# Optimization experiments

Measured on AMD Instinct MI355X. Metric: run time of the kernel, lower is better.

The kernel has to match this reference:

```python
import jax, jax.numpy as jnp
import numpy as np

B, T, E, D, G = 64, 64, 2048, 4096, 8
H3 = 3 * D  # gru projects deter -> 3*deter (reset, cand, update)
EPS = 1e-4  # Norm default eps


def _rms(x, scale):
    # Norm impl='rms': x * rsqrt(mean(x^2, -1) + eps) * scale
    return x * (jax.lax.rsqrt((x * x).mean(-1, keepdims=True) + EPS) * scale)


def setup_inputs() -> dict:
    key = jax.random.key(0)
    ks = jax.random.split(key, 4)
    x = jax.random.normal(ks[0], (B, T, E), jnp.float32)
    deter0 = jax.random.normal(ks[1], (B, D), jnp.float32)
    # dense in-projection: concat(deter, x) -> D, rms norm + silu
    W_in = jax.random.normal(ks[2], (D + E, D), jnp.float32) * (1.0 / np.sqrt(D + E))
    b_in = jnp.zeros((D,), jnp.float32)
    scale_in = jnp.ones((D,), jnp.float32)
    # BlockLinear D -> 3D with G groups; weight (G, D/G, 3D/G), per-block rms scales
    W_blk = jax.random.normal(ks[3], (G, D // G, H3 // G), jnp.float32) * (1.0 / np.sqrt(D // G))
    b_blk = jnp.zeros((H3,), jnp.float32)
    scale_blk = jnp.ones((G, H3 // G), jnp.float32)
    return dict(x=x, deter0=deter0, W_in=W_in, b_in=b_in, scale_in=scale_in,
                W_blk=W_blk, b_blk=b_blk, scale_blk=scale_blk)


def reference(x, deter0, W_in, b_in, scale_in, W_blk, b_blk, scale_blk):
    def step(deter, x_t):
        h = jnp.concatenate([deter, x_t], -1)                # [B, D+E]
        y = jax.nn.silu(_rms(h @ W_in + b_in, scale_in))     # [B, D]
        # block-diagonal GEMM: '...ki,kio->...ko' as in BlockLinear._layer
        z = jnp.einsum('bgi,gio->bgo', y.reshape(B, G, D // G), W_blk)
        z = z.reshape(B, H3) + b_blk
        # block_norm=True: per-block rms over each of the G contiguous chunks
        z = _rms(z.reshape(B, G, H3 // G), scale_blk).reshape(B, H3)
        reset, cand, update = jnp.split(z, 3, -1)
        reset = jax.nn.sigmoid(reset)
        cand = jnp.tanh(reset * cand)
        update = jax.nn.sigmoid(update - 1.0)
        deter = update * cand + (1.0 - update) * deter
        return deter, deter

    _, deters = jax.lax.scan(step, deter0, jnp.swapaxes(x, 0, 1))  # scan over T
    return jnp.swapaxes(deters, 0, 1)  # [B, T, D]
```

## Files before the change

### kernel.cpp

```cpp
#include <hip/hip_runtime.h>

typedef unsigned short u16;
typedef unsigned int u32;
typedef __bf16 bfx8 __attribute__((ext_vector_type(8)));
typedef float f32x4 __attribute__((ext_vector_type(4)));

constexpr int BB = 64;
constexpr int TT = 64;
constexpr int EE = 2048;
constexpr int DD = 4096;
constexpr int GG = 8;
constexpr int H3 = 3 * DD;
constexpr int CH = H3 / GG;
constexpr float EPSf = 1e-4f;

static __device__ __forceinline__ u16 f2bf(float f) {
  u32 u = __builtin_bit_cast(u32, f);
  u32 r = (u + 0x7fffu + ((u >> 16) & 1u)) >> 16;
  return (u16)r;
}
static __device__ __forceinline__ float bf2f(u16 h) {
  return __builtin_bit_cast(float, (u32)h << 16);
}


__global__ void __launch_bounds__(256) k_f2b(const float* __restrict__ in,
                                             u16* __restrict__ out, int n4) {
  int i = blockIdx.x * 256 + threadIdx.x;
  int stride = gridDim.x * 256;
  for (; i < n4; i += stride) {
    float4 v = ((const float4*)in)[i];
    uint2 o;
    o.x = (u32)f2bf(v.x) | ((u32)f2bf(v.y) << 16);
    o.y = (u32)f2bf(v.z) | ((u32)f2bf(v.w) << 16);
    ((uint2*)out)[i] = o;
  }
}

__global__ void __launch_bounds__(256) k_initdet(const float* __restrict__ d0,
                                                 float* __restrict__ dF,
                                                 u16* __restrict__ dB, int n4) {
  int i = blockIdx.x * 256 + threadIdx.x;
  if (i < n4) {
    float4 v = ((const float4*)d0)[i];
    ((float4*)dF)[i] = v;
    uint2 o;
    o.x = (u32)f2bf(v.x) | ((u32)f2bf(v.y) << 16);
    o.y = (u32)f2bf(v.z) | ((u32)f2bf(v.w) << 16);
    ((uint2*)dB)[i] = o;
  }
}

__global__ void __launch_bounds__(256) k_transpose_f2b(const float* __restrict__ in,
                                                       u16* __restrict__ out,
                                                       int R, int C) {
  __shared__ float tile[32][33];
  size_t base = (size_t)blockIdx.z * R * C;
  in += base; out += base;
  int tx = threadIdx.x & 31, ty = threadIdx.x >> 5;
  int r0 = blockIdx.y * 32, c0 = blockIdx.x * 32;
#pragma unroll
  for (int i = 0; i < 4; i++) {
    int rr = ty * 4 + i;
    tile[rr][tx] = in[(size_t)(r0 + rr) * C + (c0 + tx)];
  }
  __syncthreads();
#pragma unroll
  for (int i = 0; i < 4; i++) {
    int cc = ty * 4 + i;
    out[(size_t)(c0 + cc) * R + (r0 + tx)] = f2bf(tile[tx][cc]);
  }
}

constexpr int P1_LS = 72;
constexpr int P1_BUF = 128 * P1_LS;

__global__ void __launch_bounds__(256) k_p1(const u16* __restrict__ A,
                                            const u16* __restrict__ B,
                                            const float* __restrict__ bias,
                                            u16* __restrict__ C) {
  __shared__ u16 As[2 * P1_BUF];
  __shared__ u16 Bs[2 * P1_BUF];
  const int tid = threadIdx.x;
  const int m0 = blockIdx.y * 128, n0 = blockIdx.x * 128;
  const int w = tid >> 6, lane = tid & 63;
  const int wr = w >> 1, wc = w & 1;
  const int lr = lane & 15, lk = (lane >> 4) * 8, rq = (lane >> 4) * 4;
  const int srow = tid >> 3, scol = (tid & 7) * 8;
  const u16* Ag = A + (size_t)(m0 + srow) * EE + scol;
  const u16* Bg = B + (size_t)(n0 + srow) * (DD + EE) + scol;

  f32x4 acc[4][4] = {};
  uint4 ra[4], rb[4];
#pragma unroll
  for (int i = 0; i < 4; i++) {
    ra[i] = *(const uint4*)(Ag + (size_t)32 * i * EE);
    rb[i] = *(const uint4*)(Bg + (size_t)32 * i * (DD + EE));
  }

  for (int kt = 0; kt < 32; ++kt) {
    const int p = kt & 1;
    u16* ab = As + p * P1_BUF;
    u16* bb = Bs + p * P1_BUF;
#pragma unroll
    for (int i = 0; i < 4; i++) {
      *(uint4*)&ab[(srow + 32 * i) * P1_LS + scol] = ra[i];
      *(uint4*)&bb[(srow + 32 * i) * P1_LS + scol] = rb[i];
    }
    __syncthreads();
    if (kt < 31) {
      const int ko = (kt + 1) * 64;
#pragma unroll
      for (int i = 0; i < 4; i++) {
        ra[i] = *(const uint4*)(Ag + (size_t)32 * i * EE + ko);
        rb[i] = *(const uint4*)(Bg + (size_t)32 * i * (DD + EE) + ko);
      }
    }
#pragma unroll
    for (int kk = 0; kk < 64; kk += 32) {
      bfx8 av[4], bv[4];
#pragma unroll
      for (int mi = 0; mi < 4; mi++)
        av[mi] = *(const bfx8*)&ab[(wr * 64 + mi * 16 + lr) * P1_LS + kk + lk];
#pragma unroll
      for (int ni = 0; ni < 4; ni++)
        bv[ni] = *(const bfx8*)&bb[(wc * 64 + ni * 16 + lr) * P1_LS + kk + lk];
#pragma unroll
      for (int mi = 0; mi < 4; mi++)
#pragma unroll
        for (int ni = 0; ni < 4; ni++)
          acc[mi][ni] = __builtin_amdgcn_mfma_f32_16x16x32_bf16(av[mi], bv[ni], acc[mi][ni], 0, 0, 0);
    }
  }

#pragma unroll
  for (int mi = 0; mi < 4; mi++) {
#pragma unroll
    for (int ni = 0; ni < 4; ni++) {
      const int n = n0 + wc * 64 + ni * 16 + lr;
      const float bias_v = bias[n];
#pragma unroll
      for (int r = 0; r < 4; r++) {
        const int m = m0 + wr * 64 + mi * 16 + rq + r;
        C[(size_t)m * DD + n] = f2bf(acc[mi][ni][r] + bias_v);
      }
    }
  }
}

constexpr int LSA = 136;
constexpr int ABUF = 64 * LSA;

__global__ void __launch_bounds__(512) kA(const u16* __restrict__ dB,
                                          const u16* __restrict__ WT,
                                          float* __restrict__ part) {
  __shared__ u16 As[2 * ABUF];
  __shared__ u16 Bs[2 * ABUF];
  const int tid = threadIdx.x;
  const int n0 = blockIdx.x * 64;
  const int k0 = blockIdx.y * 1024;
  const int w = tid >> 6, lane = tid & 63;
  const int wr = w >> 1, wc = w & 1;
  const int lr = lane & 15, lk = (lane >> 4) * 8, rq = (lane >> 4) * 4;
  const int r0s = tid >> 4, s0 = (tid & 15) * 8;
  const int r1s = r0s + 32;
  const u16* Ag0 = dB + (size_t)r0s * DD + k0 + s0;
  const u16* Ag1 = dB + (size_t)r1s * DD + k0 + s0;
  const u16* Bg0 = WT + (size_t)(n0 + r0s) * (DD + EE) + k0 + s0;
  const u16* Bg1 = WT + (size_t)(n0 + r1s) * (DD + EE) + k0 + s0;
  const int d0 = r0s * LSA + s0, d1 = r1s * LSA + s0;

  f32x4 acc[2] = {};
  uint4 ra0 = *(const uint4*)(Ag0);
  uint4 ra1 = *(const uint4*)(Ag1);
  uint4 rb0 = *(const uint4*)(Bg0);
  uint4 rb1 = *(const uint4*)(Bg1);

  for (int kt = 0; kt < 8; ++kt) {
    const int p = kt & 1;
    u16* ab = As + p * ABUF;
    u16* bb = Bs + p * ABUF;
    *(uint4*)&ab[d0] = ra0;
    *(uint4*)&ab[d1] = ra1;
    *(uint4*)&bb[d0] = rb0;
    *(uint4*)&bb[d1] = rb1;
    __syncthreads();
    if (kt < 7) {
      const int ko = (kt + 1) * 128;
      ra0 = *(const uint4*)(Ag0 + ko);
      ra1 = *(const uint4*)(Ag1 + ko);
      rb0 = *(const uint4*)(Bg0 + ko);
      rb1 = *(const uint4*)(Bg1 + ko);
    }
#pragma unroll
    for (int kk = 0; kk < 128; kk += 32) {
      bfx8 av = *(const bfx8*)&ab[(wr * 16 + lr) * LSA + kk + lk];
#pragma unroll
      for (int ni = 0; ni < 2; ni++) {
        bfx8 bv = *(const bfx8*)&bb[(wc * 32 + ni * 16 + lr) * LSA + kk + lk];
        acc[ni] = __builtin_amdgcn_mfma_f32_16x16x32_bf16(av, bv, acc[ni], 0, 0, 0);
      }
    }
  }

  float* Pp = part + (size_t)blockIdx.y * BB * DD;
#pragma unroll
  for (int ni = 0; ni < 2; ni++)
#pragma unroll
    for (int r = 0; r < 4; r++)
      Pp[(size_t)(wr * 16 + rq + r) * DD + n0 + wc * 32 + ni * 16 + lr] = acc[ni][r];
}

__global__ void __launch_bounds__(256) kB(const float* __restrict__ part,
                                          const u16* __restrict__ Xproj,
                                          const float* __restrict__ scale_in,
                                          u16* __restrict__ ybf, int t) {
  const int b = blockIdx.x, tid = threadIdx.x;
  const int w = tid >> 6, lane = tid & 63;
  __shared__ float sred[4];
  const u16* xp = Xproj + ((size_t)b * TT + t) * DD + tid * 16;
  const float* pb = part + (size_t)b * DD + tid * 16;
  float v[16];
  uint4 x0 = *(const uint4*)(xp);
  uint4 x1 = *(const uint4*)(xp + 8);
#pragma unroll
  for (int j = 0; j < 8; j++) v[j] = bf2f(((const u16*)&x0)[j]);
#pragma unroll
  for (int j = 0; j < 8; j++) v[8 + j] = bf2f(((const u16*)&x1)[j]);
#pragma unroll
  for (int kc = 0; kc < 4; kc++) {
    const float* p = pb + (size_t)kc * BB * DD;
#pragma unroll
    for (int j4 = 0; j4 < 4; j4++) {
      float4 q = *(const float4*)(p + j4 * 4);
      v[j4 * 4 + 0] += q.x; v[j4 * 4 + 1] += q.y;
      v[j4 * 4 + 2] += q.z; v[j4 * 4 + 3] += q.w;
    }
  }
  float ss = 0.f;
#pragma unroll
  for (int j = 0; j < 16; j++) ss += v[j] * v[j];
#pragma unroll
  for (int o = 32; o > 0; o >>= 1) ss += __shfl_down(ss, o);
  if (lane == 0) sred[w] = ss;
  __syncthreads();
  const float r = rsqrtf((sred[0] + sred[1] + sred[2] + sred[3]) / (float)DD + EPSf);
  const float* sc = scale_in + tid * 16;
  uint2 o0, o1;
  u32* po = (u32*)&o0;
#pragma unroll
  for (int j = 0; j < 4; j++) {
    float a = v[2 * j] * r * sc[2 * j];
    float bq = v[2 * j + 1] * r * sc[2 * j + 1];
    a = a / (1.f + __expf(-a)); bq = bq / (1.f + __expf(-bq));
    po[j & 1] = (u32)f2bf(a) | ((u32)f2bf(bq) << 16);
    if (j == 1) *(uint2*)(ybf + (size_t)b * DD + tid * 16) = o0;
  }
  *(uint2*)(ybf + (size_t)b * DD + tid * 16 + 4) = o0;
  u32 pk[8];
#pragma unroll
  for (int j = 0; j < 8; j++) {
    float a = v[2 * j] * r * sc[2 * j];
    float bq = v[2 * j + 1] * r * sc[2 * j + 1];
    a = a / (1.f + __expf(-a)); bq = bq / (1.f + __expf(-bq));
    pk[j] = (u32)f2bf(a) | ((u32)f2bf(bq) << 16);
  }
  uint4 w0 = make_uint4(pk[0], pk[1], pk[2], pk[3]);
  uint4 w1 = make_uint4(pk[4], pk[5], pk[6], pk[7]);
  *(uint4*)(ybf + (size_t)b * DD + tid * 16) = w0;
  *(uint4*)(ybf + (size_t)b * DD + tid * 16 + 8) = w1;
}

constexpr int LSC2 = 72;
constexpr int CBUF = 64 * LSC2;

__global__ void __launch_bounds__(256) kC(const u16* __restrict__ ybf,
                                          const u16* __restrict__ WbT,
                                          const float* __restrict__ b_blk,
                                          float* __restrict__ zbuf,
                                          float* __restrict__ zsq) {
  __shared__ u16 As[2 * CBUF];
  __shared__ u16 Bs[2 * CBUF];
  const int tid = threadIdx.x;
  const int wg = blockIdx.x;
  const int n0g = wg * 64;
  const int g = n0g / CH, nl = n0g % CH;
  const int w = tid >> 6, lane = tid & 63;
  const int lr = lane & 15, lk = (lane >> 4) * 8, rq = (lane >> 4) * 4;
  const int srow = tid >> 2, sc = (tid & 3) * 8;
  const u16* Arow = ybf + (size_t)srow * DD + g * (DD / GG) + sc;
  const u16* Brow = WbT + ((size_t)g * CH + nl + srow) * (DD / GG) + sc;
  const int dA = srow * LSC2 + sc;

  f32x4 acc[4] = {};
  uint4 ra0 = *(const uint4*)(Arow);
  uint4 ra1 = *(const uint4*)(Arow + 32);
  uint4 rb0 = *(const uint4*)(Brow);
  uint4 rb1 = *(const uint4*)(Brow + 32);

  for (int kt = 0; kt < 8; ++kt) {
    const int p = kt & 1;
    u16* ab = As + p * CBUF;
    u16* bb = Bs + p * CBUF;
    *(uint4*)&ab[dA] = ra0;
    *(uint4*)&ab[dA + 32] = ra1;
    *(uint4*)&bb[dA] = rb0;
    *(uint4*)&bb[dA + 32] = rb1;
    __syncthreads();
    if (kt < 7) {
      const int ko = (kt + 1) * 64;
      ra0 = *(const uint4*)(Arow + ko);
      ra1 = *(const uint4*)(Arow + ko + 32);
      rb0 = *(const uint4*)(Brow + ko);
      rb1 = *(const uint4*)(Brow + ko + 32);
    }
#pragma unroll
    for (int kk = 0; kk < 64; kk += 32) {
      bfx8 av = *(const bfx8*)&ab[(w * 16 + lr) * LSC2 + kk + lk];
#pragma unroll
      for (int ni = 0; ni < 4; ni++) {
        bfx8 bv = *(const bfx8*)&bb[(ni * 16 + lr) * LSC2 + kk + lk];
        acc[ni] = __builtin_amdgcn_mfma_f32_16x16x32_bf16(av, bv, acc[ni], 0, 0, 0);
      }
    }
  }

  float sq[4] = {0.f, 0.f, 0.f, 0.f};
#pragma unroll
  for (int ni = 0; ni < 4; ni++) {
    const int n = n0g + ni * 16 + lr;
    const float bias_v = b_blk[n];
#pragma unroll
    for (int r = 0; r < 4; r++) {
      const float zv = acc[ni][r] + bias_v;
      zbuf[(size_t)(w * 16 + rq + r) * H3 + n] = zv;
      sq[r] += zv * zv;
    }
  }
#pragma unroll
  for (int o = 1; o < 16; o <<= 1) {
#pragma unroll
    for (int r = 0; r < 4; r++) sq[r] += __shfl_xor(sq[r], o);
  }
  if (lr == 0) {
#pragma unroll
    for (int r = 0; r < 4; r++) zsq[(size_t)wg * 64 + w * 16 + rq + r] = sq[r];
  }
}

__global__ void __launch_bounds__(256) kD(const float* __restrict__ zbuf,
                                          const float* __restrict__ zsq,
                                          const float* __restrict__ sblk,
                                          float* __restrict__ dF,
                                          u16* __restrict__ dB,
                                          float* __restrict__ out, int t) {
  const int wg = blockIdx.x, tid = threadIdx.x;
  const int b = wg >> 2, s = wg & 3;
  __shared__ float sred[8];
  if (tid < 8) {
    float ssq = 0.f;
    const int j0 = tid * 24;
#pragma unroll
    for (int j = 0; j < 24; j++) ssq += zsq[(size_t)(j0 + j) * 64 + b];
    sred[tid] = rsqrtf(ssq / (float)CH + EPSf);
  }
  __syncthreads();
  const int d0 = s * 1024 + tid * 4;
  const float* zr = zbuf + (size_t)b * H3;
  float4 z0 = *(const float4*)(zr + d0);
  float4 z1 = *(const float4*)(zr + DD + d0);
  float4 z2 = *(const float4*)(zr + 2 * DD + d0);
  float4 dold = *(const float4*)(dF + (size_t)b * DD + d0);
  const float rsA = sred[d0 / CH];
  const float rsB = sred[(DD + d0) / CH];
  const float rsC = sred[(2 * DD + d0) / CH];
  float dn[4];
  const float* z0p = (const float*)&z0;
  const float* z1p = (const float*)&z1;
  const float* z2p = (const float*)&z2;
  const float* dop = (const float*)&dold;
#pragma unroll
  for (int e = 0; e < 4; e++) {
    const int dd = d0 + e;
    const float a0 = z0p[e] * rsA * sblk[dd];
    const float a1 = z1p[e] * rsB * sblk[DD + dd];
    const float a2 = z2p[e] * rsC * sblk[2 * DD + dd];
    const float reset = 1.f / (1.f + __expf(-a0));
    const float cand = tanhf(reset * a1);
    const float upd = 1.f / (1.f + __expf(-(a2 - 1.f)));
    dn[e] = upd * cand + (1.f - upd) * dop[e];
  }
  *(float4*)(dF + (size_t)b * DD + d0) = make_float4(dn[0], dn[1], dn[2], dn[3]);
  uint2 o;
  o.x = (u32)f2bf(dn[0]) | ((u32)f2bf(dn[1]) << 16);
  o.y = (u32)f2bf(dn[2]) | ((u32)f2bf(dn[3]) << 16);
  *(uint2*)(dB + (size_t)b * DD + d0) = o;
  *(float4*)(out + ((size_t)b * TT + t) * DD + d0) = make_float4(dn[0], dn[1], dn[2], dn[3]);
}


extern "C" void kernel_launch(void* const* d_in, const int* in_sizes, int n_in,
                              void* d_out, int out_size, void* d_ws, size_t ws_size,
                              hipStream_t stream) {
  (void)in_sizes; (void)n_in; (void)out_size; (void)ws_size;
  const float* x         = (const float*)d_in[0];
  const float* deter0    = (const float*)d_in[1];
  const float* W_in      = (const float*)d_in[2];
  const float* b_in      = (const float*)d_in[3];
  const float* scale_in  = (const float*)d_in[4];
  const float* W_blk     = (const float*)d_in[5];
  const float* b_blk     = (const float*)d_in[6];
  const float* scale_blk = (const float*)d_in[7];
  float* out = (float*)d_out;

  char* ws = (char*)d_ws;
  size_t off = 0;
  auto alloc = [&](size_t bytes) -> void* {
    void* p = ws + off;
    off += (bytes + 255) & ~(size_t)255;
    return p;
  };
  u16*   WT    = (u16*)alloc((size_t)DD * (DD + EE) * 2);
  u16*   WbT   = (u16*)alloc((size_t)GG * CH * (DD / GG) * 2);
  u16*   Xproj = (u16*)alloc((size_t)BB * TT * DD * 2);
  float* dF    = (float*)alloc((size_t)BB * DD * 4);
  u16*   dB    = (u16*)alloc((size_t)BB * DD * 2);
  char* scratch = (char*)alloc((size_t)BB * TT * EE * 2);
  u16*   xbf  = (u16*)scratch;
  float* part = (float*)scratch;
  size_t o2 = (size_t)4 * BB * DD * 4;
  u16*   ybf  = (u16*)(scratch + o2);
  o2 += (size_t)BB * DD * 2;
  float* zbuf = (float*)(scratch + o2);
  o2 += (size_t)BB * H3 * 4;
  float* zsq  = (float*)(scratch + o2);

  k_f2b<<<dim3(2048), dim3(256), 0, stream>>>(x, xbf, BB * TT * EE / 4);
  k_transpose_f2b<<<dim3(DD / 32, (DD + EE) / 32, 1), dim3(256), 0, stream>>>(W_in, WT, DD + EE, DD);
  k_transpose_f2b<<<dim3(CH / 32, (DD / GG) / 32, GG), dim3(256), 0, stream>>>(W_blk, WbT, DD / GG, CH);
  k_initdet<<<dim3(BB * DD / 4 / 256), dim3(256), 0, stream>>>(deter0, dF, dB, BB * DD / 4);

  k_p1<<<dim3(DD / 128, BB * TT / 128), dim3(256), 0, stream>>>(
      xbf, WT + DD, b_in, Xproj);

  for (int t = 0; t < TT; t++) {
    kA<<<dim3(64, 4), dim3(512), 0, stream>>>(dB, WT, part);
    kB<<<dim3(BB), dim3(256), 0, stream>>>(part, Xproj, scale_in, ybf, t);
    kC<<<dim3(192), dim3(256), 0, stream>>>(ybf, WbT, b_blk, zbuf, zsq);
    kD<<<dim3(256), dim3(256), 0, stream>>>(zbuf, zsq, scale_blk, dF, dB, out, t);
  }
}
```

Baseline: 1.999 ms.

## Fuse recurrent step kernels pairwise using in-kernel grid barriers

```diff
diff --git a/kernel.cpp b/kernel.cpp
--- a/kernel.cpp
+++ b/kernel.cpp
@@ -2,6 +2,7 @@
 
 typedef unsigned short u16;
 typedef unsigned int u32;
+typedef unsigned long long u64;
 typedef __bf16 bfx8 __attribute__((ext_vector_type(8)));
 typedef float f32x4 __attribute__((ext_vector_type(4)));
 
@@ -21,6 +22,35 @@
 }
 static __device__ __forceinline__ float bf2f(u16 h) {
   return __builtin_bit_cast(float, (u32)h << 16);
+}
+
+static __device__ __forceinline__ uint2 ld_dev2(const void* p) {
+  u64 v = __hip_atomic_load((const u64*)p, __ATOMIC_RELAXED, __HIP_MEMORY_SCOPE_AGENT);
+  uint2 r; r.x = (u32)v; r.y = (u32)(v >> 32);
+  return r;
+}
+static __device__ __forceinline__ float ld_devf(const float* p) {
+  return __hip_atomic_load(p, __ATOMIC_RELAXED, __HIP_MEMORY_SCOPE_AGENT);
+}
+static __device__ __forceinline__ void st_devf(float* p, float v) {
+  __hip_atomic_store(p, v, __ATOMIC_RELAXED, __HIP_MEMORY_SCOPE_AGENT);
+}
+static __device__ __forceinline__ float2 u2f2(uint2 v) {
+  float2 r;
+  r.x = __builtin_bit_cast(float, v.x);
+  r.y = __builtin_bit_cast(float, v.y);
+  return r;
+}
+
+static __device__ __forceinline__ void gbar(int* cnt, int target) {
+  __syncthreads();
+  if (threadIdx.x == 0) {
+    __hip_atomic_fetch_add(cnt, 1, __ATOMIC_RELAXED, __HIP_MEMORY_SCOPE_AGENT);
+    while (__hip_atomic_load(cnt, __ATOMIC_RELAXED, __HIP_MEMORY_SCOPE_AGENT) < target)
+      __builtin_amdgcn_s_sleep(2);
+  }
+  __syncthreads();
+  asm volatile("" ::: "memory");
 }
 
 
@@ -49,6 +79,11 @@
     o.y = (u32)f2bf(v.z) | ((u32)f2bf(v.w) << 16);
     ((uint2*)dB)[i] = o;
   }
+}
+
+__global__ void __launch_bounds__(256) k_zero(int* __restrict__ p, int n) {
+  int i = blockIdx.x * 256 + threadIdx.x;
+  if (i < n) p[i] = 0;
 }
 
 __global__ void __launch_bounds__(256) k_transpose_f2b(const float* __restrict__ in,
@@ -151,251 +186,276 @@
 constexpr int LSA = 136;
 constexpr int ABUF = 64 * LSA;
 
-__global__ void __launch_bounds__(512) kA(const u16* __restrict__ dB,
-                                          const u16* __restrict__ WT,
-                                          float* __restrict__ part) {
+__global__ void __launch_bounds__(512) kAB(const u16* __restrict__ dB,
+                                           const u16* __restrict__ WT,
+                                           const u16* __restrict__ Xproj,
+                                           const float* __restrict__ scale_in,
+                                           float* __restrict__ part,
+                                           u16* __restrict__ ybf,
+                                           int t, int* bar) {
   __shared__ u16 As[2 * ABUF];
   __shared__ u16 Bs[2 * ABUF];
-  const int tid = threadIdx.x;
-  const int n0 = blockIdx.x * 64;
-  const int k0 = blockIdx.y * 1024;
-  const int w = tid >> 6, lane = tid & 63;
-  const int wr = w >> 1, wc = w & 1;
-  const int lr = lane & 15, lk = (lane >> 4) * 8, rq = (lane >> 4) * 4;
-  const int r0s = tid >> 4, s0 = (tid & 15) * 8;
-  const int r1s = r0s + 32;
-  const u16* Ag0 = dB + (size_t)r0s * DD + k0 + s0;
-  const u16* Ag1 = dB + (size_t)r1s * DD + k0 + s0;
-  const u16* Bg0 = WT + (size_t)(n0 + r0s) * (DD + EE) + k0 + s0;
-  const u16* Bg1 = WT + (size_t)(n0 + r1s) * (DD + EE) + k0 + s0;
-  const int d0 = r0s * LSA + s0, d1 = r1s * LSA + s0;
-
-  f32x4 acc[2] = {};
-  uint4 ra0 = *(const uint4*)(Ag0);
-  uint4 ra1 = *(const uint4*)(Ag1);
-  uint4 rb0 = *(const uint4*)(Bg0);
-  uint4 rb1 = *(const uint4*)(Bg1);
-
-  for (int kt = 0; kt < 8; ++kt) {
-    const int p = kt & 1;
-    u16* ab = As + p * ABUF;
-    u16* bb = Bs + p * ABUF;
-    *(uint4*)&ab[d0] = ra0;
-    *(uint4*)&ab[d1] = ra1;
-    *(uint4*)&bb[d0] = rb0;
-    *(uint4*)&bb[d1] = rb1;
+  __shared__ float sred[8];
+  __shared__ u16 occupancy_pad[8192];
+  const int wg = blockIdx.x, tid = threadIdx.x;
+  if ((int)blockIdx.y == -1) occupancy_pad[0] = 1;
+
+  {
+    const int n0 = (wg & 63) * 64;
+    const int k0 = (wg >> 6) * 1024;
+    const int w = tid >> 6, lane = tid & 63;
+    const int wr = w >> 1, wc = w & 1;
+    const int lr = lane & 15, lk = (lane >> 4) * 8, rq = (lane >> 4) * 4;
+    const int r0s = tid >> 4, s0 = (tid & 15) * 8;
+    const u16* Ag0 = dB + (size_t)r0s * DD + k0 + s0;
+    const u16* Ag1 = dB + (size_t)(r0s + 32) * DD + k0 + s0;
+    const u16* Bg0 = WT + (size_t)(n0 + r0s) * (DD + EE) + k0 + s0;
+    const u16* Bg1 = WT + (size_t)(n0 + r0s + 32) * (DD + EE) + k0 + s0;
+    const int d0 = r0s * LSA + s0, d1 = (r0s + 32) * LSA + s0;
+    u16* A0 = As;        u16* B0 = Bs;
+    u16* A1 = As + ABUF; u16* B1 = Bs + ABUF;
+
+    f32x4 acc[2] = {};
+    uint4 ea0 = *(const uint4*)(Ag0),      ea1 = *(const uint4*)(Ag1);
+    uint4 eb0 = *(const uint4*)(Bg0),      eb1 = *(const uint4*)(Bg1);
+    uint4 oa0 = *(const uint4*)(Ag0 + 128), oa1 = *(const uint4*)(Ag1 + 128);
+    uint4 ob0 = *(const uint4*)(Bg0 + 128), ob1 = *(const uint4*)(Bg1 + 128);
+
+#pragma unroll
+    for (int it = 0; it < 4; ++it) {
+      *(uint4*)&A0[d0] = ea0; *(uint4*)&A0[d1] = ea1;
+      *(uint4*)&B0[d0] = eb0; *(uint4*)&B0[d1] = eb1;
+      __syncthreads();
+      if (it < 3) {
+        const int ko = (2 * it + 2) * 128;
+        ea0 = *(const uint4*)(Ag0 + ko); ea1 = *(const uint4*)(Ag1 + ko);
+        eb0 = *(const uint4*)(Bg0 + ko); eb1 = *(const uint4*)(Bg1 + ko);
+      }
+#pragma unroll
+      for (int kk = 0; kk < 128; kk += 32) {
+        bfx8 av = *(const bfx8*)&A0[(wr * 16 + lr) * LSA + kk + lk];
+#pragma unroll
+        for (int ni = 0; ni < 2; ni++) {
+          bfx8 bv = *(const bfx8*)&B0[(wc * 32 + ni * 16 + lr) * LSA + kk + lk];
+          acc[ni] = __builtin_amdgcn_mfma_f32_16x16x32_bf16(av, bv, acc[ni], 0, 0, 0);
+        }
+      }
+      *(uint4*)&A1[d0] = oa0; *(uint4*)&A1[d1] = oa1;
+      *(uint4*)&B1[d0] = ob0; *(uint4*)&B1[d1] = ob1;
+      __syncthreads();
+      if (it < 3) {
+        const int ko = (2 * it + 3) * 128;
+        oa0 = *(const uint4*)(Ag0 + ko); oa1 = *(const uint4*)(Ag1 + ko);
+        ob0 = *(const uint4*)(Bg0 + ko); ob1 = *(const uint4*)(Bg1 + ko);
+      }
+#pragma unroll
+      for (int kk = 0; kk < 128; kk += 32) {
+        bfx8 av = *(const bfx8*)&A1[(wr * 16 + lr) * LSA + kk + lk];
+#pragma unroll
+        for (int ni = 0; ni < 2; ni++) {
+          bfx8 bv = *(const bfx8*)&B1[(wc * 32 + ni * 16 + lr) * LSA + kk + lk];
+          acc[ni] = __builtin_amdgcn_mfma_f32_16x16x32_bf16(av, bv, acc[ni], 0, 0, 0);
+        }
+      }
+    }
+
+    float* Pp = part + (size_t)(wg >> 6) * BB * DD;
+#pragma unroll
+    for (int ni = 0; ni < 2; ni++)
+#pragma unroll
+      for (int r = 0; r < 4; r++)
+        st_devf(&Pp[(size_t)(wr * 16 + rq + r) * DD + n0 + wc * 32 + ni * 16 + lr],
+                acc[ni][r]);
+  }
+
+  gbar(bar, 256);
+
+  if (wg < BB) {
+    const int b = wg;
+    const int w = tid >> 6, lane = tid & 63;
+    const u16* xp = Xproj + ((size_t)b * TT + t) * DD + tid * 8;
+    const float* pb = part + (size_t)b * DD + tid * 8;
+    float v[8];
+    uint4 x0 = *(const uint4*)(xp);
+#pragma unroll
+    for (int j = 0; j < 8; j++) v[j] = bf2f(((const u16*)&x0)[j]);
+#pragma unroll
+    for (int kc = 0; kc < 4; kc++) {
+      const float* p = pb + (size_t)kc * BB * DD;
+#pragma unroll
+      for (int j2 = 0; j2 < 4; j2++) {
+        float2 q = u2f2(ld_dev2(p + j2 * 2));
+        v[j2 * 2] += q.x;
+        v[j2 * 2 + 1] += q.y;
+      }
+    }
+    float ss = 0.f;
+#pragma unroll
+    for (int j = 0; j < 8; j++) ss += v[j] * v[j];
+#pragma unroll
+    for (int o = 32; o > 0; o >>= 1) ss += __shfl_down(ss, o);
+    if (lane == 0) sred[w] = ss;
     __syncthreads();
-    if (kt < 7) {
-      const int ko = (kt + 1) * 128;
-      ra0 = *(const uint4*)(Ag0 + ko);
-      ra1 = *(const uint4*)(Ag1 + ko);
-      rb0 = *(const uint4*)(Bg0 + ko);
-      rb1 = *(const uint4*)(Bg1 + ko);
-    }
-#pragma unroll
-    for (int kk = 0; kk < 128; kk += 32) {
-      bfx8 av = *(const bfx8*)&ab[(wr * 16 + lr) * LSA + kk + lk];
-#pragma unroll
-      for (int ni = 0; ni < 2; ni++) {
-        bfx8 bv = *(const bfx8*)&bb[(wc * 32 + ni * 16 + lr) * LSA + kk + lk];
-        acc[ni] = __builtin_amdgcn_mfma_f32_16x16x32_bf16(av, bv, acc[ni], 0, 0, 0);
-      }
-    }
-  }
-
-  float* Pp = part + (size_t)blockIdx.y * BB * DD;
-#pragma unroll
-  for (int ni = 0; ni < 2; ni++)
-#pragma unroll
-    for (int r = 0; r < 4; r++)
-      Pp[(size_t)(wr * 16 + rq + r) * DD + n0 + wc * 32 + ni * 16 + lr] = acc[ni][r];
-}
-
-__global__ void __launch_bounds__(256) kB(const float* __restrict__ part,
-                                          const u16* __restrict__ Xproj,
-                                          const float* __restrict__ scale_in,
-                                          u16* __restrict__ ybf, int t) {
-  const int b = blockIdx.x, tid = threadIdx.x;
-  const int w = tid >> 6, lane = tid & 63;
-  __shared__ float sred[4];
-  const u16* xp = Xproj + ((size_t)b * TT + t) * DD + tid * 16;
-  const float* pb = part + (size_t)b * DD + tid * 16;
-  float v[16];
-  uint4 x0 = *(const uint4*)(xp);
-  uint4 x1 = *(const uint4*)(xp + 8);
-#pragma unroll
-  for (int j = 0; j < 8; j++) v[j] = bf2f(((const u16*)&x0)[j]);
-#pragma unroll
-  for (int j = 0; j < 8; j++) v[8 + j] = bf2f(((const u16*)&x1)[j]);
-#pragma unroll
-  for (int kc = 0; kc < 4; kc++) {
-    const float* p = pb + (size_t)kc * BB * DD;
-#pragma unroll
-    for (int j4 = 0; j4 < 4; j4++) {
-      float4 q = *(const float4*)(p + j4 * 4);
-      v[j4 * 4 + 0] += q.x; v[j4 * 4 + 1] += q.y;
-      v[j4 * 4 + 2] += q.z; v[j4 * 4 + 3] += q.w;
-    }
-  }
-  float ss = 0.f;
-#pragma unroll
-  for (int j = 0; j < 16; j++) ss += v[j] * v[j];
-#pragma unroll
-  for (int o = 32; o > 0; o >>= 1) ss += __shfl_down(ss, o);
-  if (lane == 0) sred[w] = ss;
-  __syncthreads();
-  const float r = rsqrtf((sred[0] + sred[1] + sred[2] + sred[3]) / (float)DD + EPSf);
-  const float* sc = scale_in + tid * 16;
-  uint2 o0, o1;
-  u32* po = (u32*)&o0;
-#pragma unroll
-  for (int j = 0; j < 4; j++) {
-    float a = v[2 * j] * r * sc[2 * j];
-    float bq = v[2 * j + 1] * r * sc[2 * j + 1];
-    a = a / (1.f + __expf(-a)); bq = bq / (1.f + __expf(-bq));
-    po[j & 1] = (u32)f2bf(a) | ((u32)f2bf(bq) << 16);
-    if (j == 1) *(uint2*)(ybf + (size_t)b * DD + tid * 16) = o0;
-  }
-  *(uint2*)(ybf + (size_t)b * DD + tid * 16 + 4) = o0;
-  u32 pk[8];
-#pragma unroll
-  for (int j = 0; j < 8; j++) {
-    float a = v[2 * j] * r * sc[2 * j];
-    float bq = v[2 * j + 1] * r * sc[2 * j + 1];
-    a = a / (1.f + __expf(-a)); bq = bq / (1.f + __expf(-bq));
-    pk[j] = (u32)f2bf(a) | ((u32)f2bf(bq) << 16);
-  }
-  uint4 w0 = make_uint4(pk[0], pk[1], pk[2], pk[3]);
-  uint4 w1 = make_uint4(pk[4], pk[5], pk[6], pk[7]);
-  *(uint4*)(ybf + (size_t)b * DD + tid * 16) = w0;
-  *(uint4*)(ybf + (size_t)b * DD + tid * 16 + 8) = w1;
+    float tot = 0.f;
+#pragma unroll
+    for (int i = 0; i < 8; i++) tot += sred[i];
+    const float r = rsqrtf(tot / (float)DD + EPSf);
+    const float* sc = scale_in + tid * 8;
+    u32 pk[4];
+#pragma unroll
+    for (int j = 0; j < 4; j++) {
+      float a = v[2 * j] * r * sc[2 * j];
+      float bq = v[2 * j + 1] * r * sc[2 * j + 1];
+      a = a / (1.f + __expf(-a));
+      bq = bq / (1.f + __expf(-bq));
+      pk[j] = (u32)f2bf(a) | ((u32)f2bf(bq) << 16);
+    }
+    *(uint4*)(ybf + (size_t)b * DD + tid * 8) = make_uint4(pk[0], pk[1], pk[2], pk[3]);
+  }
 }
 
 constexpr int LSC2 = 72;
 constexpr int CBUF = 64 * LSC2;
 
-__global__ void __launch_bounds__(256) kC(const u16* __restrict__ ybf,
-                                          const u16* __restrict__ WbT,
-                                          const float* __restrict__ b_blk,
-                                          float* __restrict__ zbuf,
-                                          float* __restrict__ zsq) {
+__global__ void __launch_bounds__(512) kCD(const u16* __restrict__ ybf,
+                                           const u16* __restrict__ WbT,
+                                           const float* __restrict__ b_blk,
+                                           const float* __restrict__ sblk,
+                                           float* __restrict__ zbuf,
+                                           float* __restrict__ zsq,
+                                           float* __restrict__ dF,
+                                           u16* __restrict__ dBout,
+                                           float* __restrict__ out,
+                                           int t, int* bar) {
   __shared__ u16 As[2 * CBUF];
   __shared__ u16 Bs[2 * CBUF];
-  const int tid = threadIdx.x;
-  const int wg = blockIdx.x;
-  const int n0g = wg * 64;
-  const int g = n0g / CH, nl = n0g % CH;
-  const int w = tid >> 6, lane = tid & 63;
-  const int lr = lane & 15, lk = (lane >> 4) * 8, rq = (lane >> 4) * 4;
-  const int srow = tid >> 2, sc = (tid & 3) * 8;
-  const u16* Arow = ybf + (size_t)srow * DD + g * (DD / GG) + sc;
-  const u16* Brow = WbT + ((size_t)g * CH + nl + srow) * (DD / GG) + sc;
-  const int dA = srow * LSC2 + sc;
-
-  f32x4 acc[4] = {};
-  uint4 ra0 = *(const uint4*)(Arow);
-  uint4 ra1 = *(const uint4*)(Arow + 32);
-  uint4 rb0 = *(const uint4*)(Brow);
-  uint4 rb1 = *(const uint4*)(Brow + 32);
-
-  for (int kt = 0; kt < 8; ++kt) {
-    const int p = kt & 1;
-    u16* ab = As + p * CBUF;
-    u16* bb = Bs + p * CBUF;
-    *(uint4*)&ab[dA] = ra0;
-    *(uint4*)&ab[dA + 32] = ra1;
-    *(uint4*)&bb[dA] = rb0;
-    *(uint4*)&bb[dA + 32] = rb1;
+  __shared__ float sred[8];
+  __shared__ u16 occupancy_pad[24576];
+  const int wg = blockIdx.x, tid = threadIdx.x;
+  if ((int)blockIdx.y == -1) occupancy_pad[0] = 1;
+
+  {
+    const int n0g = wg * 64;
+    const int g = wg / 24, nl = n0g - g * CH;
+    const int w = tid >> 6, lane = tid & 63;
+    const int wr = w >> 1, wc = w & 1;
+    const int lr = lane & 15, lk = (lane >> 4) * 8, rq = (lane >> 4) * 4;
+    const int srow = tid >> 3, sc = (tid & 7) * 8;
+    const u16* Arow = ybf + (size_t)srow * DD + g * 512 + sc;
+    const u16* Brow = WbT + ((size_t)g * CH + nl + srow) * 512 + sc;
+    const int dA = srow * LSC2 + sc;
+    u16* A0 = As;        u16* B0 = Bs;
+    u16* A1 = As + CBUF; u16* B1 = Bs + CBUF;
+
+    f32x4 acc[2] = {};
+    uint4 ea = *(const uint4*)(Arow),      eb = *(const uint4*)(Brow);
+    uint4 oa = *(const uint4*)(Arow + 64), ob = *(const uint4*)(Brow + 64);
+
+#pragma unroll
+    for (int it = 0; it < 4; ++it) {
+      *(uint4*)&A0[dA] = ea; *(uint4*)&B0[dA] = eb;
+      __syncthreads();
+      if (it < 3) {
+        const int ko = (2 * it + 2) * 64;
+        ea = *(const uint4*)(Arow + ko); eb = *(const uint4*)(Brow + ko);
+      }
+#pragma unroll
+      for (int kk = 0; kk < 64; kk += 32) {
+        bfx8 av = *(const bfx8*)&A0[(wr * 16 + lr) * LSC2 + kk + lk];
+#pragma unroll
+        for (int ni = 0; ni < 2; ni++) {
+          bfx8 bv = *(const bfx8*)&B0[(wc * 32 + ni * 16 + lr) * LSC2 + kk + lk];
+          acc[ni] = __builtin_amdgcn_mfma_f32_16x16x32_bf16(av, bv, acc[ni], 0, 0, 0);
+        }
+      }
+      *(uint4*)&A1[dA] = oa; *(uint4*)&B1[dA] = ob;
+      __syncthreads();
+      if (it < 3) {
+        const int ko = (2 * it + 3) * 64;
+        oa = *(const uint4*)(Arow + ko); ob = *(const uint4*)(Brow + ko);
+      }
+#pragma unroll
+      for (int kk = 0; kk < 64; kk += 32) {
+        bfx8 av = *(const bfx8*)&A1[(wr * 16 + lr) * LSC2 + kk + lk];
+#pragma unroll
+        for (int ni = 0; ni < 2; ni++) {
+          bfx8 bv = *(const bfx8*)&B1[(wc * 32 + ni * 16 + lr) * LSC2 + kk + lk];
+          acc[ni] = __builtin_amdgcn_mfma_f32_16x16x32_bf16(av, bv, acc[ni], 0, 0, 0);
+        }
+      }
+    }
+
+    float sq[4] = {0.f, 0.f, 0.f, 0.f};
+#pragma unroll
+    for (int ni = 0; ni < 2; ni++) {
+      const int n = n0g + wc * 32 + ni * 16 + lr;
+      const float bias_v = b_blk[n];
+#pragma unroll
+      for (int r = 0; r < 4; r++) {
+        const float zv = acc[ni][r] + bias_v;
+        st_devf(&zbuf[(size_t)(wr * 16 + rq + r) * H3 + n], zv);
+        sq[r] += zv * zv;
+      }
+    }
+#pragma unroll
+    for (int o = 1; o < 16; o <<= 1) {
+#pragma unroll
+      for (int r = 0; r < 4; r++) sq[r] += __shfl_xor(sq[r], o);
+    }
+    if (lr == 0) {
+#pragma unroll
+      for (int r = 0; r < 4; r++)
+        st_devf(&zsq[(size_t)wg * 128 + wc * 64 + wr * 16 + rq + r], sq[r]);
+    }
+  }
+
+  gbar(bar, 192);
+
+  if (wg < 128) {
+    const int b = wg >> 1, s = wg & 1;
+    if (tid < 8) {
+      float ssq = 0.f;
+      const int c0 = tid * 24;
+#pragma unroll
+      for (int j = 0; j < 24; j++) {
+        const size_t base = (size_t)(c0 + j) * 128;
+        ssq += ld_devf(&zsq[base + b]) + ld_devf(&zsq[base + 64 + b]);
+      }
+      sred[tid] = rsqrtf(ssq / (float)CH + EPSf);
+    }
     __syncthreads();
-    if (kt < 7) {
-      const int ko = (kt + 1) * 64;
-      ra0 = *(const uint4*)(Arow + ko);
-      ra1 = *(const uint4*)(Arow + ko + 32);
-      rb0 = *(const uint4*)(Brow + ko);
-      rb1 = *(const uint4*)(Brow + ko + 32);
-    }
-#pragma unroll
-    for (int kk = 0; kk < 64; kk += 32) {
-      bfx8 av = *(const bfx8*)&ab[(w * 16 + lr) * LSC2 + kk + lk];
-#pragma unroll
-      for (int ni = 0; ni < 4; ni++) {
-        bfx8 bv = *(const bfx8*)&bb[(ni * 16 + lr) * LSC2 + kk + lk];
-        acc[ni] = __builtin_amdgcn_mfma_f32_16x16x32_bf16(av, bv, acc[ni], 0, 0, 0);
-      }
-    }
-  }
-
-  float sq[4] = {0.f, 0.f, 0.f, 0.f};
-#pragma unroll
-  for (int ni = 0; ni < 4; ni++) {
-    const int n = n0g + ni * 16 + lr;
-    const float bias_v = b_blk[n];
-#pragma unroll
-    for (int r = 0; r < 4; r++) {
-      const float zv = acc[ni][r] + bias_v;
-      zbuf[(size_t)(w * 16 + rq + r) * H3 + n] = zv;
-      sq[r] += zv * zv;
-    }
-  }
-#pragma unroll
-  for (int o = 1; o < 16; o <<= 1) {
-#pragma unroll
-    for (int r = 0; r < 4; r++) sq[r] += __shfl_xor(sq[r], o);
-  }
-  if (lr == 0) {
-#pragma unroll
-    for (int r = 0; r < 4; r++) zsq[(size_t)wg * 64 + w * 16 + rq + r] = sq[r];
-  }
-}
-
-__global__ void __launch_bounds__(256) kD(const float* __restrict__ zbuf,
-                                          const float* __restrict__ zsq,
-                                          const float* __restrict__ sblk,
-                                          float* __restrict__ dF,
-                                          u16* __restrict__ dB,
-                                          float* __restrict__ out, int t) {
-  const int wg = blockIdx.x, tid = threadIdx.x;
-  const int b = wg >> 2, s = wg & 3;
-  __shared__ float sred[8];
-  if (tid < 8) {
-    float ssq = 0.f;
-    const int j0 = tid * 24;
-#pragma unroll
-    for (int j = 0; j < 24; j++) ssq += zsq[(size_t)(j0 + j) * 64 + b];
-    sred[tid] = rsqrtf(ssq / (float)CH + EPSf);
-  }
-  __syncthreads();
-  const int d0 = s * 1024 + tid * 4;
-  const float* zr = zbuf + (size_t)b * H3;
-  float4 z0 = *(const float4*)(zr + d0);
-  float4 z1 = *(const float4*)(zr + DD + d0);
-  float4 z2 = *(const float4*)(zr + 2 * DD + d0);
-  float4 dold = *(const float4*)(dF + (size_t)b * DD + d0);
-  const float rsA = sred[d0 / CH];
-  const float rsB = sred[(DD + d0) / CH];
-  const float rsC = sred[(2 * DD + d0) / CH];
-  float dn[4];
-  const float* z0p = (const float*)&z0;
-  const float* z1p = (const float*)&z1;
-  const float* z2p = (const float*)&z2;
-  const float* dop = (const float*)&dold;
-#pragma unroll
-  for (int e = 0; e < 4; e++) {
-    const int dd = d0 + e;
-    const float a0 = z0p[e] * rsA * sblk[dd];
-    const float a1 = z1p[e] * rsB * sblk[DD + dd];
-    const float a2 = z2p[e] * rsC * sblk[2 * DD + dd];
-    const float reset = 1.f / (1.f + __expf(-a0));
-    const float cand = tanhf(reset * a1);
-    const float upd = 1.f / (1.f + __expf(-(a2 - 1.f)));
-    dn[e] = upd * cand + (1.f - upd) * dop[e];
-  }
-  *(float4*)(dF + (size_t)b * DD + d0) = make_float4(dn[0], dn[1], dn[2], dn[3]);
-  uint2 o;
-  o.x = (u32)f2bf(dn[0]) | ((u32)f2bf(dn[1]) << 16);
-  o.y = (u32)f2bf(dn[2]) | ((u32)f2bf(dn[3]) << 16);
-  *(uint2*)(dB + (size_t)b * DD + d0) = o;
-  *(float4*)(out + ((size_t)b * TT + t) * DD + d0) = make_float4(dn[0], dn[1], dn[2], dn[3]);
+    const int d0 = s * 2048 + tid * 4;
+    const float* zr = zbuf + (size_t)b * H3;
+    float2 z0a = u2f2(ld_dev2(zr + d0)),          z0b = u2f2(ld_dev2(zr + d0 + 2));
+    float2 z1a = u2f2(ld_dev2(zr + DD + d0)),     z1b = u2f2(ld_dev2(zr + DD + d0 + 2));
+    float2 z2a = u2f2(ld_dev2(zr + 2 * DD + d0)), z2b = u2f2(ld_dev2(zr + 2 * DD + d0 + 2));
+    float4 dold = *(const float4*)(dF + (size_t)b * DD + d0);
+    const float rsA = sred[d0 / CH];
+    const float rsB = sred[(DD + d0) / CH];
+    const float rsC = sred[(2 * DD + d0) / CH];
+    float z0p[4] = {z0a.x, z0a.y, z0b.x, z0b.y};
+    float z1p[4] = {z1a.x, z1a.y, z1b.x, z1b.y};
+    float z2p[4] = {z2a.x, z2a.y, z2b.x, z2b.y};
+    const float* dop = (const float*)&dold;
+    float dn[4];
+#pragma unroll
+    for (int e = 0; e < 4; e++) {
+      const int dd = d0 + e;
+      const float a0 = z0p[e] * rsA * sblk[dd];
+      const float a1 = z1p[e] * rsB * sblk[DD + dd];
+      const float a2 = z2p[e] * rsC * sblk[2 * DD + dd];
+      const float reset = 1.f / (1.f + __expf(-a0));
+      const float cand = tanhf(reset * a1);
+      const float upd = 1.f / (1.f + __expf(-(a2 - 1.f)));
+      dn[e] = upd * cand + (1.f - upd) * dop[e];
+    }
+    *(float4*)(dF + (size_t)b * DD + d0) = make_float4(dn[0], dn[1], dn[2], dn[3]);
+    uint2 o;
+    o.x = (u32)f2bf(dn[0]) | ((u32)f2bf(dn[1]) << 16);
+    o.y = (u32)f2bf(dn[2]) | ((u32)f2bf(dn[3]) << 16);
+    *(uint2*)(dBout + (size_t)b * DD + d0) = o;
+    *(float4*)(out + ((size_t)b * TT + t) * DD + d0) = make_float4(dn[0], dn[1], dn[2], dn[3]);
+  }
 }
 
 
@@ -425,6 +485,7 @@
   u16*   Xproj = (u16*)alloc((size_t)BB * TT * DD * 2);
   float* dF    = (float*)alloc((size_t)BB * DD * 4);
   u16*   dB    = (u16*)alloc((size_t)BB * DD * 2);
+  int*   bars  = (int*)alloc((size_t)TT * 2 * 4);
   char* scratch = (char*)alloc((size_t)BB * TT * EE * 2);
   u16*   xbf  = (u16*)scratch;
   float* part = (float*)scratch;
@@ -439,14 +500,16 @@
   k_transpose_f2b<<<dim3(DD / 32, (DD + EE) / 32, 1), dim3(256), 0, stream>>>(W_in, WT, DD + EE, DD);
   k_transpose_f2b<<<dim3(CH / 32, (DD / GG) / 32, GG), dim3(256), 0, stream>>>(W_blk, WbT, DD / GG, CH);
   k_initdet<<<dim3(BB * DD / 4 / 256), dim3(256), 0, stream>>>(deter0, dF, dB, BB * DD / 4);
+  k_zero<<<dim3(1), dim3(256), 0, stream>>>(bars, TT * 2);
 
   k_p1<<<dim3(DD / 128, BB * TT / 128), dim3(256), 0, stream>>>(
       xbf, WT + DD, b_in, Xproj);
 
   for (int t = 0; t < TT; t++) {
-    kA<<<dim3(64, 4), dim3(512), 0, stream>>>(dB, WT, part);
-    kB<<<dim3(BB), dim3(256), 0, stream>>>(part, Xproj, scale_in, ybf, t);
-    kC<<<dim3(192), dim3(256), 0, stream>>>(ybf, WbT, b_blk, zbuf, zsq);
-    kD<<<dim3(256), dim3(256), 0, stream>>>(zbuf, zsq, scale_blk, dF, dB, out, t);
-  }
-}
+    kAB<<<dim3(256), dim3(512), 0, stream>>>(dB, WT, Xproj, scale_in,
+                                             part, ybf, t, bars + 2 * t);
+    kCD<<<dim3(192), dim3(512), 0, stream>>>(ybf, WbT, b_blk, scale_blk,
+                                             zbuf, zsq, dF, dB, out, t,
+                                             bars + 2 * t + 1);
+  }
+}
```

After: 2.312 ms. 1.16x slower.

## Drop register-prefetch double buffering in input-projection GEMM, remove redundant kB stores

Applied to the files above, without the earlier changes.

```diff
diff --git a/kernel.cpp b/kernel.cpp
--- a/kernel.cpp
+++ b/kernel.cpp
@@ -72,67 +72,55 @@
   }
 }
 
-constexpr int P1_LS = 72;
-constexpr int P1_BUF = 128 * P1_LS;
 
 __global__ void __launch_bounds__(256) k_p1(const u16* __restrict__ A,
                                             const u16* __restrict__ B,
                                             const float* __restrict__ bias,
                                             u16* __restrict__ C) {
-  __shared__ u16 As[2 * P1_BUF];
-  __shared__ u16 Bs[2 * P1_BUF];
+  constexpr int BK = 64, LS = BK + 8;
+  __shared__ u16 As[128 * LS];
+  __shared__ u16 Bs[128 * LS];
   const int tid = threadIdx.x;
   const int m0 = blockIdx.y * 128, n0 = blockIdx.x * 128;
   const int w = tid >> 6, lane = tid & 63;
   const int wr = w >> 1, wc = w & 1;
-  const int lr = lane & 15, lk = (lane >> 4) * 8, rq = (lane >> 4) * 4;
-  const int srow = tid >> 3, scol = (tid & 7) * 8;
-  const u16* Ag = A + (size_t)(m0 + srow) * EE + scol;
-  const u16* Bg = B + (size_t)(n0 + srow) * (DD + EE) + scol;
+  const int lr = lane & 15, lk = (lane >> 4) * 8;
 
   f32x4 acc[4][4] = {};
-  uint4 ra[4], rb[4];
-#pragma unroll
-  for (int i = 0; i < 4; i++) {
-    ra[i] = *(const uint4*)(Ag + (size_t)32 * i * EE);
-    rb[i] = *(const uint4*)(Bg + (size_t)32 * i * (DD + EE));
-  }
-
-  for (int kt = 0; kt < 32; ++kt) {
-    const int p = kt & 1;
-    u16* ab = As + p * P1_BUF;
-    u16* bb = Bs + p * P1_BUF;
-#pragma unroll
-    for (int i = 0; i < 4; i++) {
-      *(uint4*)&ab[(srow + 32 * i) * P1_LS + scol] = ra[i];
-      *(uint4*)&bb[(srow + 32 * i) * P1_LS + scol] = rb[i];
+
+  for (int kt = 0; kt < EE; kt += BK) {
+#pragma unroll
+    for (int c = tid; c < 128 * 8; c += 256) {
+      int row = c >> 3, cc = c & 7;
+      *(uint4*)&As[row * LS + cc * 8] =
+          *(const uint4*)(A + (size_t)(m0 + row) * EE + kt + cc * 8);
+    }
+#pragma unroll
+    for (int c = tid; c < 128 * 8; c += 256) {
+      int row = c >> 3, cc = c & 7;
+      *(uint4*)&Bs[row * LS + cc * 8] =
+          *(const uint4*)(B + (size_t)(n0 + row) * (DD + EE) + kt + cc * 8);
     }
     __syncthreads();
-    if (kt < 31) {
-      const int ko = (kt + 1) * 64;
-#pragma unroll
-      for (int i = 0; i < 4; i++) {
-        ra[i] = *(const uint4*)(Ag + (size_t)32 * i * EE + ko);
-        rb[i] = *(const uint4*)(Bg + (size_t)32 * i * (DD + EE) + ko);
-      }
-    }
-#pragma unroll
-    for (int kk = 0; kk < 64; kk += 32) {
+#pragma unroll
+    for (int kk = 0; kk < BK; kk += 32) {
       bfx8 av[4], bv[4];
 #pragma unroll
       for (int mi = 0; mi < 4; mi++)
-        av[mi] = *(const bfx8*)&ab[(wr * 64 + mi * 16 + lr) * P1_LS + kk + lk];
+        av[mi] = *(const bfx8*)&As[(wr * 64 + mi * 16 + lr) * LS + kk + lk];
 #pragma unroll
       for (int ni = 0; ni < 4; ni++)
-        bv[ni] = *(const bfx8*)&bb[(wc * 64 + ni * 16 + lr) * P1_LS + kk + lk];
+        bv[ni] = *(const bfx8*)&Bs[(wc * 64 + ni * 16 + lr) * LS + kk + lk];
 #pragma unroll
       for (int mi = 0; mi < 4; mi++)
 #pragma unroll
         for (int ni = 0; ni < 4; ni++)
           acc[mi][ni] = __builtin_amdgcn_mfma_f32_16x16x32_bf16(av[mi], bv[ni], acc[mi][ni], 0, 0, 0);
     }
-  }
-
+    __syncthreads();
+  }
+
+  const int rq = (lane >> 4) * 4;
 #pragma unroll
   for (int mi = 0; mi < 4; mi++) {
 #pragma unroll
@@ -224,9 +212,10 @@
   uint4 x0 = *(const uint4*)(xp);
   uint4 x1 = *(const uint4*)(xp + 8);
 #pragma unroll
-  for (int j = 0; j < 8; j++) v[j] = bf2f(((const u16*)&x0)[j]);
-#pragma unroll
-  for (int j = 0; j < 8; j++) v[8 + j] = bf2f(((const u16*)&x1)[j]);
+  for (int j = 0; j < 8; j++) {
+    v[j] = bf2f(((const u16*)&x0)[j]);
+    v[8 + j] = bf2f(((const u16*)&x1)[j]);
+  }
 #pragma unroll
   for (int kc = 0; kc < 4; kc++) {
     const float* p = pb + (size_t)kc * BB * DD;
@@ -246,29 +235,17 @@
   __syncthreads();
   const float r = rsqrtf((sred[0] + sred[1] + sred[2] + sred[3]) / (float)DD + EPSf);
   const float* sc = scale_in + tid * 16;
-  uint2 o0, o1;
-  u32* po = (u32*)&o0;
-#pragma unroll
-  for (int j = 0; j < 4; j++) {
-    float a = v[2 * j] * r * sc[2 * j];
-    float bq = v[2 * j + 1] * r * sc[2 * j + 1];
-    a = a / (1.f + __expf(-a)); bq = bq / (1.f + __expf(-bq));
-    po[j & 1] = (u32)f2bf(a) | ((u32)f2bf(bq) << 16);
-    if (j == 1) *(uint2*)(ybf + (size_t)b * DD + tid * 16) = o0;
-  }
-  *(uint2*)(ybf + (size_t)b * DD + tid * 16 + 4) = o0;
   u32 pk[8];
 #pragma unroll
   for (int j = 0; j < 8; j++) {
     float a = v[2 * j] * r * sc[2 * j];
     float bq = v[2 * j + 1] * r * sc[2 * j + 1];
-    a = a / (1.f + __expf(-a)); bq = bq / (1.f + __expf(-bq));
+    a = a / (1.f + __expf(-a));
+    bq = bq / (1.f + __expf(-bq));
     pk[j] = (u32)f2bf(a) | ((u32)f2bf(bq) << 16);
   }
-  uint4 w0 = make_uint4(pk[0], pk[1], pk[2], pk[3]);
-  uint4 w1 = make_uint4(pk[4], pk[5], pk[6], pk[7]);
-  *(uint4*)(ybf + (size_t)b * DD + tid * 16) = w0;
-  *(uint4*)(ybf + (size_t)b * DD + tid * 16 + 8) = w1;
+  *(uint4*)(ybf + (size_t)b * DD + tid * 16) = make_uint4(pk[0], pk[1], pk[2], pk[3]);
+  *(uint4*)(ybf + (size_t)b * DD + tid * 16 + 8) = make_uint4(pk[4], pk[5], pk[6], pk[7]);
 }
 
 constexpr int LSC2 = 72;
```

Measured after the change: 1.892 ms. 5.4% less time.
